# Kernel optimization log

Hardware: AMD Instinct MI355X
Metric: run time of the kernel (lower is better)

## Reference

```python
import jax, jax.numpy as jnp
import numpy as np

B, S, D, H, DH = 2, 2048, 2048, 16, 128


def _rope(t, cos, sin):
    # t: [b,s,h,dh]; pairs are consecutive elements (view(..., -1, 2) in torch)
    te = t[..., 0::2]
    to = t[..., 1::2]
    re = te * cos - to * sin
    im = te * sin + to * cos
    return jnp.stack([re, im], axis=-1).reshape(t.shape)


def setup_inputs() -> dict:
    key = jax.random.key(0)
    ks = jax.random.split(key, 5)
    inv = 1.0 / np.sqrt(D)
    x = jax.random.normal(ks[0], (B, S, D), dtype=jnp.float32)
    # standard RoPE angle table -> cos/sin of shape [1,S,1,DH//2]
    pos = jnp.arange(S, dtype=jnp.float32)[:, None]
    freqs = 1.0 / (10000.0 ** (jnp.arange(0, DH, 2, dtype=jnp.float32) / DH))
    ang = pos * freqs[None, :]
    rope_cos = jnp.cos(ang)[None, :, None, :]
    rope_sin = jnp.sin(ang)[None, :, None, :]
    Wq = jax.random.normal(ks[1], (D, D), dtype=jnp.float32) * inv
    Wk = jax.random.normal(ks[2], (D, D), dtype=jnp.float32) * inv
    Wv = jax.random.normal(ks[3], (D, D), dtype=jnp.float32) * inv
    Wo = jax.random.normal(ks[4], (D, D), dtype=jnp.float32) * inv
    return {"x": x, "rope_cos": rope_cos, "rope_sin": rope_sin,
            "Wq": Wq, "Wk": Wk, "Wv": Wv, "Wo": Wo}


def reference(x, rope_cos, rope_sin, Wq, Wk, Wv, Wo):
    b, s, d = x.shape
    scale = DH ** (-0.5)
    # nn.Linear(bias=False): y = x @ W.T
    q = (x @ Wq.T).reshape(b, s, H, DH)
    k = (x @ Wk.T).reshape(b, s, H, DH)
    v = (x @ Wv.T).reshape(b, s, H, DH)
    q = _rope(q, rope_cos[:, :s], rope_sin[:, :s])
    k = _rope(k, rope_cos[:, :s], rope_sin[:, :s])
    q = q.transpose(0, 2, 1, 3)  # bhsd
    k = k.transpose(0, 2, 1, 3)
    v = v.transpose(0, 2, 1, 3)
    # full scores needed for softmax normalizer
    scores = jnp.einsum('bhqd,bhkd->bhqk', q, k) * scale
    lse = jax.nn.logsumexp(scores, axis=-1)  # [b,h,s]
    # torch.einsum('bhss,bhsd->bhsd', softmax(scores), v) takes the DIAGONAL
    # of the softmax matrix and scales v elementwise. Replicate exactly:
    diag = jnp.einsum('bhsd,bhsd->bhs', q, k) * scale  # scores[b,h,s,s]
    w = jnp.exp(diag - lse)  # softmax(scores)[b,h,s,s]
    out = w[..., None] * v  # [b,h,s,dh]
    out = out.transpose(0, 2, 1, 3).reshape(b, s, d)
    return out @ Wo.T
```

## Files before the change

### kernel.cpp

```cpp
#include <hip/hip_runtime.h>

#define B_  2
#define S_  2048
#define D_  2048
#define H_  16
#define DH_ 128
#define NQKV 6144

typedef __bf16 bf16;
typedef __bf16 bf16x2 __attribute__((ext_vector_type(2)));
typedef __bf16 bf16x4 __attribute__((ext_vector_type(4)));
typedef __bf16 bf16x8 __attribute__((ext_vector_type(8)));
typedef float  f32x4  __attribute__((ext_vector_type(4)));

#define EXP2F(x) __builtin_amdgcn_exp2f(x)
#define LOG2F(x) __builtin_amdgcn_logf(x)

static constexpr float kQScale = 0.08838834764831845f * 1.4426950408889634f;

__device__ __forceinline__ void async16(const void* g, void* l) {
  __builtin_amdgcn_global_load_lds(
      (const __attribute__((address_space(1))) void*)g,
      (__attribute__((address_space(3))) void*)l, 16, 0, 0);
}

__global__ void cvt_bf16(const float* __restrict__ s, bf16* __restrict__ d) {
  int i = (blockIdx.x * 256 + threadIdx.x) * 4;
  float4 v = *(const float4*)(s + i);
  bf16x4 o = {(bf16)v.x, (bf16)v.y, (bf16)v.z, (bf16)v.w};
  *(bf16x4*)(d + i) = o;
}

__global__ __launch_bounds__(256, 2) void gemm_qkv(
    const bf16* __restrict__ A, const bf16* __restrict__ Bm,
    const float* __restrict__ rc, const float* __restrict__ rs,
    bf16* __restrict__ C) {
  __shared__ alignas(16) bf16 As[2][128 * 32];
  __shared__ alignas(16) bf16 Bs[2][128 * 32];
  const int tid = threadIdx.x;
  const int lane = tid & 63;
  const int wv = tid >> 6;
  const int quad = lane >> 4, c16 = lane & 15;
  const int wm = (wv >> 1) * 64, wn = (wv & 1) * 64;
  const int m0 = blockIdx.y * 128, n0 = blockIdx.x * 128;

  const bf16* ag = A  + (size_t)(m0 + (tid >> 2)) * D_ + (tid & 3) * 8;
  const bf16* bg = Bm + (size_t)(n0 + (tid >> 2)) * D_ + (tid & 3) * 8;
  char* asl = (char*)As + tid * 16;
  char* bsl = (char*)Bs + tid * 16;

  f32x4 acc[4][4] = {};
  for (int k0 = 0; k0 < D_; k0 += 64) {
    __syncthreads();
    async16(ag + k0,                 asl);
    async16(ag + k0 + 64 * D_,       asl + 4096);
    async16(ag + k0 + 32,            asl + 8192);
    async16(ag + k0 + 32 + 64 * D_,  asl + 12288);
    async16(bg + k0,                 bsl);
    async16(bg + k0 + 64 * D_,       bsl + 4096);
    async16(bg + k0 + 32,            bsl + 8192);
    async16(bg + k0 + 32 + 64 * D_,  bsl + 12288);
    __syncthreads();
#pragma unroll
    for (int half = 0; half < 2; ++half) {
      bf16x8 af[4], bfr[4];
#pragma unroll
      for (int i = 0; i < 4; ++i)
        af[i] = *(const bf16x8*)(As[half] + (wm + i * 16 + c16) * 32 + quad * 8);
#pragma unroll
      for (int j = 0; j < 4; ++j)
        bfr[j] = *(const bf16x8*)(Bs[half] + (wn + j * 16 + c16) * 32 + quad * 8);
#pragma unroll
      for (int i = 0; i < 4; ++i)
#pragma unroll
        for (int j = 0; j < 4; ++j)
          acc[i][j] = __builtin_amdgcn_mfma_f32_16x16x32_bf16(af[i], bfr[j], acc[i][j], 0, 0, 0);
    }
  }

  if (n0 < 4096) {
    const float sc = (n0 < 2048) ? kQScale : 1.0f;
#pragma unroll
    for (int i = 0; i < 4; ++i) {
      const int gmi = m0 + wm + i * 16 + quad * 4;
#pragma unroll
      for (int j = 0; j < 4; ++j) {
        const int gn = n0 + wn + j * 16 + c16;
        const int d = gn & 127;
#pragma unroll
        for (int r = 0; r < 4; ++r) {
          float v = acc[i][j][r];
          float p = __shfl_xor(v, 1);
          const int gm = gmi + r;
          const int s = gm & 2047;
          const int si = s * 64 + (d >> 1);
          float c = rc[si], sn = rs[si];
          float re = (v * c - p * sn) * sc;
          float im = (v * sn + p * c) * sc;
          if (!(lane & 1)) {
            bf16x2 o = {(bf16)re, (bf16)im};
            *(bf16x2*)(C + (size_t)gm * NQKV + gn) = o;
          }
        }
      }
    }
  } else {
#pragma unroll
    for (int i = 0; i < 4; ++i) {
      const int gmi = m0 + wm + i * 16 + quad * 4;
#pragma unroll
      for (int j = 0; j < 4; ++j) {
        const int gn = n0 + wn + j * 16 + c16;
#pragma unroll
        for (int r = 0; r < 4; ++r) {
          float v = acc[i][j][r];
          float p = __shfl_xor(v, 1);
          if (!(lane & 1)) {
            bf16x2 o = {(bf16)v, (bf16)p};
            *(bf16x2*)(C + (size_t)(gmi + r) * NQKV + gn) = o;
          }
        }
      }
    }
  }
}

__global__ __launch_bounds__(256, 2) void score_lse(
    const bf16* __restrict__ qkv,
    float* __restrict__ lse, float* __restrict__ diag) {
  __shared__ alignas(16) bf16 Qs[4 * 128 * 32];
  __shared__ alignas(16) bf16 Ks[4 * 128 * 32];
  const int tid = threadIdx.x;
  const int lane = tid & 63, wv = tid >> 6;
  const int quad = lane >> 4, c16 = lane & 15;
  const int wm = wv * 32;
  const int bh = blockIdx.y;
  const int b = bh >> 4, h = bh & 15;
  const int m0 = blockIdx.x * 128;

  const bf16* qg = qkv + (size_t)(b * 2048 + m0 + (tid >> 2)) * NQKV
                 + h * 128 + (tid & 3) * 8;
  char* ql = (char*)Qs + tid * 16;
#pragma unroll
  for (int kt = 0; kt < 4; ++kt) {
    async16(qg + kt * 32,               ql + kt * 8192);
    async16(qg + kt * 32 + (size_t)64 * NQKV, ql + kt * 8192 + 4096);
  }

  const bf16* kg = qkv + (size_t)(b * 2048 + (tid >> 2)) * NQKV
                 + 2048 + h * 128 + (tid & 3) * 8;
  char* kl = (char*)Ks + tid * 16;

  float sums[8] = {0.f, 0.f, 0.f, 0.f, 0.f, 0.f, 0.f, 0.f};

  for (int n0 = 0; n0 < S_; n0 += 128) {
    __syncthreads();
#pragma unroll
    for (int kt = 0; kt < 4; ++kt) {
      async16(kg + (size_t)n0 * NQKV + kt * 32,        kl + kt * 8192);
      async16(kg + (size_t)(n0 + 64) * NQKV + kt * 32, kl + kt * 8192 + 4096);
    }
    __syncthreads();
    f32x4 acc[2][8] = {};
#pragma unroll
    for (int kt = 0; kt < 4; ++kt) {
      bf16x8 a[2], bb[8];
#pragma unroll
      for (int i = 0; i < 2; ++i)
        a[i] = *(const bf16x8*)(Qs + kt * 4096 + (wm + i * 16 + c16) * 32 + quad * 8);
#pragma unroll
      for (int j = 0; j < 8; ++j)
        bb[j] = *(const bf16x8*)(Ks + kt * 4096 + (j * 16 + c16) * 32 + quad * 8);
#pragma unroll
      for (int i = 0; i < 2; ++i)
#pragma unroll
        for (int j = 0; j < 8; ++j)
          acc[i][j] = __builtin_amdgcn_mfma_f32_16x16x32_bf16(a[i], bb[j], acc[i][j], 0, 0, 0);
    }
    if (n0 == m0) {
#pragma unroll
      for (int i = 0; i < 2; ++i)
#pragma unroll
        for (int j = 0; j < 8; ++j)
          if (j == 2 * wv + i) {
#pragma unroll
            for (int r = 0; r < 4; ++r)
              if (c16 == quad * 4 + r) {
                int row = wm + i * 16 + quad * 4 + r;
                diag[bh * S_ + m0 + row] = acc[i][j][r];
              }
          }
    }
#pragma unroll
    for (int i = 0; i < 2; ++i)
#pragma unroll
      for (int j = 0; j < 8; ++j)
#pragma unroll
        for (int r = 0; r < 4; ++r)
          sums[i * 4 + r] += EXP2F(acc[i][j][r]);
  }

#pragma unroll
  for (int t = 0; t < 8; ++t) {
    float s = sums[t];
    s += __shfl_xor(s, 1);
    s += __shfl_xor(s, 2);
    s += __shfl_xor(s, 4);
    s += __shfl_xor(s, 8);
    if (c16 == 0) {
      int i = t >> 2, r = t & 3;
      lse[bh * S_ + m0 + wm + i * 16 + quad * 4 + r] = LOG2F(s);
    }
  }
}

__global__ void wv_mul(const bf16* __restrict__ qkv, const float* __restrict__ lse,
                       const float* __restrict__ diag, bf16* __restrict__ t) {
  int u = blockIdx.x * 256 + threadIdx.x;
  int e = u * 8;
  int m = e >> 11;
  int c = e & 2047;
  int g = ((m >> 11) * 16 + (c >> 7)) * 2048 + (m & 2047);
  float w = EXP2F(diag[g] - lse[g]);
  bf16x8 v = *(const bf16x8*)(qkv + (size_t)m * NQKV + 4096 + c);
  bf16x8 o;
#pragma unroll
  for (int r = 0; r < 8; ++r) o[r] = (bf16)((float)v[r] * w);
  ((bf16x8*)t)[u] = o;
}

__global__ __launch_bounds__(256, 2) void gemm_out(
    const bf16* __restrict__ A, const bf16* __restrict__ Bm, float* __restrict__ C) {
  __shared__ alignas(16) bf16 As[2][128 * 32];
  __shared__ alignas(16) bf16 Bs[2][128 * 32];
  const int tid = threadIdx.x;
  const int lane = tid & 63, wv = tid >> 6;
  const int quad = lane >> 4, c16 = lane & 15;
  const int wm = (wv >> 1) * 64, wn = (wv & 1) * 64;
  const int m0 = blockIdx.y * 128, n0 = blockIdx.x * 128;

  const bf16* ag = A  + (size_t)(m0 + (tid >> 2)) * D_ + (tid & 3) * 8;
  const bf16* bg = Bm + (size_t)(n0 + (tid >> 2)) * D_ + (tid & 3) * 8;
  char* asl = (char*)As + tid * 16;
  char* bsl = (char*)Bs + tid * 16;

  f32x4 acc[4][4] = {};
  for (int k0 = 0; k0 < D_; k0 += 64) {
    __syncthreads();
    async16(ag + k0,                 asl);
    async16(ag + k0 + 64 * D_,       asl + 4096);
    async16(ag + k0 + 32,            asl + 8192);
    async16(ag + k0 + 32 + 64 * D_,  asl + 12288);
    async16(bg + k0,                 bsl);
    async16(bg + k0 + 64 * D_,       bsl + 4096);
    async16(bg + k0 + 32,            bsl + 8192);
    async16(bg + k0 + 32 + 64 * D_,  bsl + 12288);
    __syncthreads();
#pragma unroll
    for (int half = 0; half < 2; ++half) {
      bf16x8 af[4], bfr[4];
#pragma unroll
      for (int i = 0; i < 4; ++i)
        af[i] = *(const bf16x8*)(As[half] + (wm + i * 16 + c16) * 32 + quad * 8);
#pragma unroll
      for (int j = 0; j < 4; ++j)
        bfr[j] = *(const bf16x8*)(Bs[half] + (wn + j * 16 + c16) * 32 + quad * 8);
#pragma unroll
      for (int i = 0; i < 4; ++i)
#pragma unroll
        for (int j = 0; j < 4; ++j)
          acc[i][j] = __builtin_amdgcn_mfma_f32_16x16x32_bf16(af[i], bfr[j], acc[i][j], 0, 0, 0);
    }
  }
#pragma unroll
  for (int i = 0; i < 4; ++i)
#pragma unroll
    for (int j = 0; j < 4; ++j)
#pragma unroll
      for (int r = 0; r < 4; ++r) {
        float v = acc[i][j][r];
        float p = __shfl_xor(v, 1);
        if (!(lane & 1)) {
          int gm = m0 + wm + i * 16 + quad * 4 + r;
          int gn = n0 + wn + j * 16 + c16;
          float2 o = {v, p};
          *(float2*)(C + (size_t)gm * D_ + gn) = o;
        }
      }
}

extern "C" void kernel_launch(void* const* d_in, const int* in_sizes, int n_in,
                              void* d_out, int out_size, void* d_ws, size_t ws_size,
                              hipStream_t stream) {
  (void)in_sizes; (void)n_in; (void)out_size; (void)ws_size;
  const float* x  = (const float*)d_in[0];
  const float* rc = (const float*)d_in[1];
  const float* rs = (const float*)d_in[2];
  const float* Wq = (const float*)d_in[3];
  const float* Wk = (const float*)d_in[4];
  const float* Wv = (const float*)d_in[5];
  const float* Wo = (const float*)d_in[6];

  char* ws = (char*)d_ws;
  bf16* xb   = (bf16*)ws;
  bf16* wqkv = (bf16*)(ws + 16777216);
  bf16* wob  = (bf16*)(ws + 16777216 + 25165824);
  bf16* qkv  = (bf16*)(ws + 16777216 + 25165824 + 8388608);
  float* lse = (float*)((char*)qkv + 50331648);
  float* dia = lse + 65536;

  cvt_bf16<<<8192, 256, 0, stream>>>(x,  xb);
  cvt_bf16<<<4096, 256, 0, stream>>>(Wq, wqkv);
  cvt_bf16<<<4096, 256, 0, stream>>>(Wk, wqkv + 4194304);
  cvt_bf16<<<4096, 256, 0, stream>>>(Wv, wqkv + 8388608);
  cvt_bf16<<<4096, 256, 0, stream>>>(Wo, wob);

  gemm_qkv<<<dim3(48, 32), 256, 0, stream>>>(xb, wqkv, rc, rs, qkv);
  score_lse<<<dim3(16, 32), 256, 0, stream>>>(qkv, lse, dia);
  wv_mul<<<4096, 256, 0, stream>>>(qkv, lse, dia, xb );
  gemm_out<<<dim3(16, 32), 256, 0, stream>>>(xb, wob, (float*)d_out);
}
```

Before: 384.4 us.

## Fuse diagonal-weight V scaling into score kernel and merge conversion launches

The elementwise wv_mul pass now runs inside the score/LSE kernel. Diagonal scores and LSE stay in shared memory, and each block scales its own 128 rows of V right after the row sums finish. The five fp32-to-bf16 conversion launches are merged into one kernel that picks its source by block index. This removes the global round trip for lse/diag and four kernel launches. In exchange, the V scaling becomes a serial tail inside the score kernel instead of a fully parallel separate pass.

```diff
diff --git a/kernel.cpp b/kernel.cpp
--- a/kernel.cpp
+++ b/kernel.cpp
@@ -24,8 +24,19 @@
       (__attribute__((address_space(3))) void*)l, 16, 0, 0);
 }
 
-__global__ void cvt_bf16(const float* __restrict__ s, bf16* __restrict__ d) {
-  int i = (blockIdx.x * 256 + threadIdx.x) * 4;
+__global__ void cvt_all(const float* __restrict__ x,  const float* __restrict__ wq,
+                        const float* __restrict__ wk, const float* __restrict__ wv,
+                        const float* __restrict__ wo,
+                        bf16* __restrict__ xb, bf16* __restrict__ wqkv,
+                        bf16* __restrict__ wob) {
+  int bid = blockIdx.x;
+  const float* s; bf16* d; int base;
+  if (bid < 8192)        { s = x;  d = xb;             base = bid; }
+  else if (bid < 12288)  { s = wq; d = wqkv;           base = bid - 8192; }
+  else if (bid < 16384)  { s = wk; d = wqkv + 4194304; base = bid - 12288; }
+  else if (bid < 20480)  { s = wv; d = wqkv + 8388608; base = bid - 16384; }
+  else                   { s = wo; d = wob;            base = bid - 20480; }
+  int i = (base * 256 + threadIdx.x) * 4;
   float4 v = *(const float4*)(s + i);
   bf16x4 o = {(bf16)v.x, (bf16)v.y, (bf16)v.z, (bf16)v.w};
   *(bf16x4*)(d + i) = o;
@@ -125,11 +136,12 @@
   }
 }
 
-__global__ __launch_bounds__(256, 2) void score_lse(
-    const bf16* __restrict__ qkv,
-    float* __restrict__ lse, float* __restrict__ diag) {
+__global__ __launch_bounds__(256, 2) void score_wv(
+    const bf16* __restrict__ qkv, bf16* __restrict__ t) {
   __shared__ alignas(16) bf16 Qs[4 * 128 * 32];
   __shared__ alignas(16) bf16 Ks[4 * 128 * 32];
+  __shared__ float diagL[128];
+  __shared__ float lseL[128];
   const int tid = threadIdx.x;
   const int lane = tid & 63, wv = tid >> 6;
   const int quad = lane >> 4, c16 = lane & 15;
@@ -143,7 +155,7 @@
   char* ql = (char*)Qs + tid * 16;
 #pragma unroll
   for (int kt = 0; kt < 4; ++kt) {
-    async16(qg + kt * 32,               ql + kt * 8192);
+    async16(qg + kt * 32,                     ql + kt * 8192);
     async16(qg + kt * 32 + (size_t)64 * NQKV, ql + kt * 8192 + 4096);
   }
 
@@ -185,10 +197,8 @@
           if (j == 2 * wv + i) {
 #pragma unroll
             for (int r = 0; r < 4; ++r)
-              if (c16 == quad * 4 + r) {
-                int row = wm + i * 16 + quad * 4 + r;
-                diag[bh * S_ + m0 + row] = acc[i][j][r];
-              }
+              if (c16 == quad * 4 + r)
+                diagL[wm + i * 16 + quad * 4 + r] = acc[i][j][r];
           }
     }
 #pragma unroll
@@ -201,32 +211,32 @@
   }
 
 #pragma unroll
-  for (int t = 0; t < 8; ++t) {
-    float s = sums[t];
+  for (int tix = 0; tix < 8; ++tix) {
+    float s = sums[tix];
     s += __shfl_xor(s, 1);
     s += __shfl_xor(s, 2);
     s += __shfl_xor(s, 4);
     s += __shfl_xor(s, 8);
     if (c16 == 0) {
-      int i = t >> 2, r = t & 3;
-      lse[bh * S_ + m0 + wm + i * 16 + quad * 4 + r] = LOG2F(s);
-    }
-  }
-}
-
-__global__ void wv_mul(const bf16* __restrict__ qkv, const float* __restrict__ lse,
-                       const float* __restrict__ diag, bf16* __restrict__ t) {
-  int u = blockIdx.x * 256 + threadIdx.x;
-  int e = u * 8;
-  int m = e >> 11;
-  int c = e & 2047;
-  int g = ((m >> 11) * 16 + (c >> 7)) * 2048 + (m & 2047);
-  float w = EXP2F(diag[g] - lse[g]);
-  bf16x8 v = *(const bf16x8*)(qkv + (size_t)m * NQKV + 4096 + c);
-  bf16x8 o;
-#pragma unroll
-  for (int r = 0; r < 8; ++r) o[r] = (bf16)((float)v[r] * w);
-  ((bf16x8*)t)[u] = o;
+      int i = tix >> 2, r = tix & 3;
+      lseL[wm + i * 16 + quad * 4 + r] = LOG2F(s);
+    }
+  }
+
+  __syncthreads();
+  const int row = tid >> 1, ch = tid & 1;
+  const float w = EXP2F(diagL[row] - lseL[row]);
+  const size_t grow = (size_t)(b * 2048 + m0 + row);
+  const bf16* vsrc = qkv + grow * NQKV + 4096 + h * 128 + ch * 64;
+  bf16* tdst = t + grow * 2048 + h * 128 + ch * 64;
+#pragma unroll
+  for (int c = 0; c < 8; ++c) {
+    bf16x8 vv = *(const bf16x8*)(vsrc + c * 8);
+    bf16x8 oo;
+#pragma unroll
+    for (int r = 0; r < 8; ++r) oo[r] = (bf16)((float)vv[r] * w);
+    *(bf16x8*)(tdst + c * 8) = oo;
+  }
 }
 
 __global__ __launch_bounds__(256, 2) void gemm_out(
@@ -306,17 +316,9 @@
   bf16* wqkv = (bf16*)(ws + 16777216);
   bf16* wob  = (bf16*)(ws + 16777216 + 25165824);
   bf16* qkv  = (bf16*)(ws + 16777216 + 25165824 + 8388608);
-  float* lse = (float*)((char*)qkv + 50331648);
-  float* dia = lse + 65536;
-
-  cvt_bf16<<<8192, 256, 0, stream>>>(x,  xb);
-  cvt_bf16<<<4096, 256, 0, stream>>>(Wq, wqkv);
-  cvt_bf16<<<4096, 256, 0, stream>>>(Wk, wqkv + 4194304);
-  cvt_bf16<<<4096, 256, 0, stream>>>(Wv, wqkv + 8388608);
-  cvt_bf16<<<4096, 256, 0, stream>>>(Wo, wob);
-
+
+  cvt_all<<<24576, 256, 0, stream>>>(x, Wq, Wk, Wv, Wo, xb, wqkv, wob);
   gemm_qkv<<<dim3(48, 32), 256, 0, stream>>>(xb, wqkv, rc, rs, qkv);
-  score_lse<<<dim3(16, 32), 256, 0, stream>>>(qkv, lse, dia);
-  wv_mul<<<4096, 256, 0, stream>>>(qkv, lse, dia, xb );
+  score_wv<<<dim3(16, 32), 256, 0, stream>>>(qkv, xb );
   gemm_out<<<dim3(16, 32), 256, 0, stream>>>(xb, wob, (float*)d_out);
 }
```

After: 367.3 us. 1.05x faster.
